# Kernel optimization log

Measured on AMD Instinct MI355X. Metric: run time of the kernel, lower is better.

## Reference

```python
import jax, jax.numpy as jnp
from jax import lax
import numpy as np

# Guide bandwidths (sigma^2) for the cross-bilateral weights.
SIGMA_ALBEDO = 0.01
SIGMA_NORMAL = 0.1
SIGMA_DEPTH = 0.1
EPS = 1e-10

B, H, W = 4, 720, 1280
WIN = 11


def setup_inputs() -> dict:
    key = jax.random.key(0)
    k1, k2, k3, k4 = jax.random.split(key, 4)
    inp = jax.random.normal(k1, (B, 3, H, W), dtype=jnp.float32)
    albedo = jax.random.uniform(k2, (B, 3, H, W), dtype=jnp.float32)
    normal = jax.random.normal(k3, (B, 3, H, W), dtype=jnp.float32)
    normal = normal / (jnp.linalg.norm(normal, axis=1, keepdims=True) + EPS)
    depth = jax.random.uniform(k4, (B, 1, H, W), dtype=jnp.float32)
    return {"input": inp, "albedo": albedo, "normal": normal,
            "depth": depth, "win_size": WIN}


def _cross_bilateral(inp, albedo, normal, depth, win_size):
    pad = win_size // 2
    b, c, h, w = inp.shape

    def pad4(x):
        return jnp.pad(x, ((0, 0), (0, 0), (pad, pad), (pad, pad)), mode="edge")

    ip, ap, np_, dp = pad4(inp), pad4(albedo), pad4(normal), pad4(depth)

    # All (dy, dx) taps in the window, scanned to keep memory O(B*C*H*W).
    offs = jnp.asarray([(dy, dx) for dy in range(win_size) for dx in range(win_size)],
                       dtype=jnp.int32)

    def tap(carry, off):
        acc, wsum = carry
        dy, dx = off[0], off[1]

        def sl(x):
            return lax.dynamic_slice(x, (0, 0, dy, dx), (b, x.shape[1], h, w))

        dA = jnp.sum((albedo - sl(ap)) ** 2, axis=1, keepdims=True)  # [B,1,H,W]
        dN = jnp.sum((normal - sl(np_)) ** 2, axis=1, keepdims=True)
        dD = (depth - sl(dp)) ** 2
        wgt = jnp.exp(-(dA / SIGMA_ALBEDO + dN / SIGMA_NORMAL + dD / SIGMA_DEPTH))
        return (acc + wgt * sl(ip), wsum + wgt), None

    init = (jnp.zeros_like(inp), jnp.zeros((b, 1, h, w), dtype=inp.dtype))
    (acc, wsum), _ = lax.scan(tap, init, offs)
    return acc / jnp.maximum(wsum, EPS)


def reference(input, albedo, normal, depth, win_size):
    return _cross_bilateral(input, albedo, normal, depth, win_size)
```

## Files before the change

### kernel.cpp

```cpp
#include <hip/hip_runtime.h>
#include <math.h>


#define HH   720
#define WW   1280
#define PAD  5
#define WIN  11
#define TW   32
#define TH   16
#define HALO_W (TW + 2 * PAD)
#define HALO_H (TH + 2 * PAD)

typedef _Float16 h2 __attribute__((ext_vector_type(2)));

__device__ __forceinline__ unsigned int pkh2(float a, float b) {
    return __builtin_bit_cast(unsigned int, __builtin_amdgcn_cvt_pkrtz(a, b));
}

__device__ __forceinline__ float dot2acc(h2 d, float acc) {
#if __has_builtin(__builtin_amdgcn_fdot2)
    return __builtin_amdgcn_fdot2(d, d, acc, false);
#else
    float x = (float)d.x, y = (float)d.y;
    return fmaf(x, x, fmaf(y, y, acc));
#endif
}

struct C8 { h2 c0, c1, c2, c3; };

__device__ __forceinline__ C8 unpackC(uint4 g) {
    C8 c;
    c.c0 = __builtin_bit_cast(h2, g.x);
    c.c1 = __builtin_bit_cast(h2, g.y);
    c.c2 = __builtin_bit_cast(h2, g.z);
    c.c3 = __builtin_bit_cast(h2, g.w);
    return c;
}

__device__ __forceinline__ void tap(const C8& c, uint4 g, float4 iv, float4& acc) {
    h2 d0 = __builtin_bit_cast(h2, g.x) - c.c0;
    h2 d1 = __builtin_bit_cast(h2, g.y) - c.c1;
    h2 d2 = __builtin_bit_cast(h2, g.z) - c.c2;
    h2 d3 = __builtin_bit_cast(h2, g.w) - c.c3;
    float e = dot2acc(d0, dot2acc(d1, dot2acc(d2, dot2acc(d3, 0.f))));
    float w = __builtin_amdgcn_exp2f(-e);
    acc.x = fmaf(w, iv.x, acc.x);
    acc.y = fmaf(w, iv.y, acc.y);
    acc.z = fmaf(w, iv.z, acc.z);
    acc.w += w;
}

__global__ __launch_bounds__(256, 4)
void xbilateral_kernel(const float* __restrict__ inp,
                       const float* __restrict__ alb,
                       const float* __restrict__ nrm,
                       const float* __restrict__ dep,
                       float* __restrict__ out)
{
    __shared__ uint4  sG[HALO_H][HALO_W];
    __shared__ float4 sI[HALO_H][HALO_W];

    const int tid = threadIdx.x;
    const int lx  = tid & 31;
    const int ly  = tid >> 5;
    const int bx0 = blockIdx.x * TW;
    const int by0 = blockIdx.y * TH;
    const int b   = blockIdx.z;

    const float kA = 12.01122406f;
    const float kN = 3.79828255f;

    const size_t plane = (size_t)HH * WW;
    const float* albB = alb + (size_t)b * 3 * plane;
    const float* nrmB = nrm + (size_t)b * 3 * plane;
    const float* inpB = inp + (size_t)b * 3 * plane;
    const float* depB = dep + (size_t)b * plane;

    for (int idx = tid; idx < HALO_H * HALO_W; idx += 256) {
        int r = idx / HALO_W;
        int c = idx - r * HALO_W;
        int gy = by0 + r - PAD; gy = min(max(gy, 0), HH - 1);
        int gx = bx0 + c - PAD; gx = min(max(gx, 0), WW - 1);
        size_t o = (size_t)gy * WW + gx;
        float a0 = albB[o], a1 = albB[plane + o], a2 = albB[2 * plane + o];
        float n0 = nrmB[o], n1 = nrmB[plane + o], n2 = nrmB[2 * plane + o];
        float i0 = inpB[o], i1 = inpB[plane + o], i2 = inpB[2 * plane + o];
        float d0 = depB[o];
        sG[r][c] = make_uint4(pkh2(a0 * kA, a1 * kA),
                              pkh2(a2 * kA, d0 * kN),
                              pkh2(n0 * kN, n1 * kN),
                              pkh2(n2 * kN, 0.f));
        sI[r][c] = make_float4(i0, i1, i2, 0.f);
    }
    __syncthreads();

    const int pyA = 2 * ly;
    const C8 cA = unpackC(sG[pyA + PAD][lx + PAD]);
    const C8 cB = unpackC(sG[pyA + 1 + PAD][lx + PAD]);

    float4 accA = make_float4(0.f, 0.f, 0.f, 0.f);
    float4 accB = make_float4(0.f, 0.f, 0.f, 0.f);

    {
        const uint4*  rg = &sG[pyA][lx];
        const float4* ri = &sI[pyA][lx];
#pragma unroll
        for (int dx = 0; dx < WIN; ++dx)
            tap(cA, rg[dx], ri[dx], accA);
    }
    for (int wy = 1; wy <= 10; ++wy) {
        const uint4*  rg = &sG[pyA + wy][lx];
        const float4* ri = &sI[pyA + wy][lx];
#pragma unroll
        for (int dx = 0; dx < WIN; ++dx) {
            uint4  g  = rg[dx];
            float4 iv = ri[dx];
            tap(cA, g, iv, accA);
            tap(cB, g, iv, accB);
        }
    }
    {
        const uint4*  rg = &sG[pyA + 11][lx];
        const float4* ri = &sI[pyA + 11][lx];
#pragma unroll
        for (int dx = 0; dx < WIN; ++dx)
            tap(cB, rg[dx], ri[dx], accB);
    }

    const int ox  = bx0 + lx;
    const int oyA = by0 + pyA;
    const int oyB = oyA + 1;
    float* outB = out + (size_t)b * 3 * plane;
    float invA = 1.0f / fmaxf(accA.w, 1e-10f);
    float invB = 1.0f / fmaxf(accB.w, 1e-10f);
    size_t oA = (size_t)oyA * WW + ox;
    size_t oB = (size_t)oyB * WW + ox;
    outB[oA]             = accA.x * invA;
    outB[plane + oA]     = accA.y * invA;
    outB[2 * plane + oA] = accA.z * invA;
    outB[oB]             = accB.x * invB;
    outB[plane + oB]     = accB.y * invB;
    outB[2 * plane + oB] = accB.z * invB;
}

extern "C" void kernel_launch(void* const* d_in, const int* in_sizes, int n_in,
                              void* d_out, int out_size, void* d_ws, size_t ws_size,
                              hipStream_t stream) {
    const float* inp = (const float*)d_in[0];
    const float* alb = (const float*)d_in[1];
    const float* nrm = (const float*)d_in[2];
    const float* dep = (const float*)d_in[3];
    float* out = (float*)d_out;

    dim3 grid(WW / TW, HH / TH, 4);
    dim3 block(256);
    xbilateral_kernel<<<grid, block, 0, stream>>>(inp, alb, nrm, dep, out);
}
```

Before: 214.9 us.

## Compute four output rows per thread with 32x32 tiles and fp16 input staging

Doubles the tile height to 32 and has each thread compute four vertically adjacent output pixels. Each loaded shared-memory row of guide and input taps is reused across up to four accumulators, which cuts LDS traffic per tap. The input colour is now stored as packed fp16 in LDS, which halves its footprint but reduces the precision of the filtered values. 720 is not a multiple of 32, so the last tile row is partly wasted. The larger register footprint lowers the occupancy target in launch bounds from 4 to 3.

```diff
diff --git a/kernel.cpp b/kernel.cpp
--- a/kernel.cpp
+++ b/kernel.cpp
@@ -7,58 +7,36 @@
 #define PAD  5
 #define WIN  11
 #define TW   32
-#define TH   16
-#define HALO_W (TW + 2 * PAD)
-#define HALO_H (TH + 2 * PAD)
+#define TH   32
+#define HW2  42
 
 typedef _Float16 h2 __attribute__((ext_vector_type(2)));
 
-__device__ __forceinline__ unsigned int pkh2(float a, float b) {
-    return __builtin_bit_cast(unsigned int, __builtin_amdgcn_cvt_pkrtz(a, b));
+__device__ __forceinline__ unsigned pk2(float a, float b) {
+    unsigned lo = __builtin_bit_cast(unsigned short, (_Float16)a);
+    unsigned hi = __builtin_bit_cast(unsigned short, (_Float16)b);
+    return lo | (hi << 16);
 }
 
-__device__ __forceinline__ float dot2acc(h2 d, float acc) {
+__device__ __forceinline__ float fdot2(h2 a, h2 b, float c) {
 #if __has_builtin(__builtin_amdgcn_fdot2)
-    return __builtin_amdgcn_fdot2(d, d, acc, false);
+    return __builtin_amdgcn_fdot2(a, b, c, false);
 #else
-    float x = (float)d.x, y = (float)d.y;
-    return fmaf(x, x, fmaf(y, y, acc));
+    return fmaf((float)a.x, (float)b.x, fmaf((float)a.y, (float)b.y, c));
 #endif
 }
 
-struct C8 { h2 c0, c1, c2, c3; };
+__device__ __forceinline__ h2 bch2(unsigned u) { return __builtin_bit_cast(h2, u); }
 
-__device__ __forceinline__ C8 unpackC(uint4 g) {
-    C8 c;
-    c.c0 = __builtin_bit_cast(h2, g.x);
-    c.c1 = __builtin_bit_cast(h2, g.y);
-    c.c2 = __builtin_bit_cast(h2, g.z);
-    c.c3 = __builtin_bit_cast(h2, g.w);
-    return c;
-}
-
-__device__ __forceinline__ void tap(const C8& c, uint4 g, float4 iv, float4& acc) {
-    h2 d0 = __builtin_bit_cast(h2, g.x) - c.c0;
-    h2 d1 = __builtin_bit_cast(h2, g.y) - c.c1;
-    h2 d2 = __builtin_bit_cast(h2, g.z) - c.c2;
-    h2 d3 = __builtin_bit_cast(h2, g.w) - c.c3;
-    float e = dot2acc(d0, dot2acc(d1, dot2acc(d2, dot2acc(d3, 0.f))));
-    float w = __builtin_amdgcn_exp2f(-e);
-    acc.x = fmaf(w, iv.x, acc.x);
-    acc.y = fmaf(w, iv.y, acc.y);
-    acc.z = fmaf(w, iv.z, acc.z);
-    acc.w += w;
-}
-
-__global__ __launch_bounds__(256, 4)
+__global__ __launch_bounds__(256, 3)
 void xbilateral_kernel(const float* __restrict__ inp,
                        const float* __restrict__ alb,
                        const float* __restrict__ nrm,
                        const float* __restrict__ dep,
                        float* __restrict__ out)
 {
-    __shared__ uint4  sG[HALO_H][HALO_W];
-    __shared__ float4 sI[HALO_H][HALO_W];
+    __shared__ uint4 sG[HW2][HW2];
+    __shared__ uint2 sI[HW2][HW2];
 
     const int tid = threadIdx.x;
     const int lx  = tid & 31;
@@ -76,71 +54,86 @@
     const float* inpB = inp + (size_t)b * 3 * plane;
     const float* depB = dep + (size_t)b * plane;
 
-    for (int idx = tid; idx < HALO_H * HALO_W; idx += 256) {
-        int r = idx / HALO_W;
-        int c = idx - r * HALO_W;
+    for (int idx = tid; idx < HW2 * HW2; idx += 256) {
+        int r = idx / HW2;
+        int c = idx - r * HW2;
         int gy = by0 + r - PAD; gy = min(max(gy, 0), HH - 1);
         int gx = bx0 + c - PAD; gx = min(max(gx, 0), WW - 1);
         size_t o = (size_t)gy * WW + gx;
-        float a0 = albB[o], a1 = albB[plane + o], a2 = albB[2 * plane + o];
-        float n0 = nrmB[o], n1 = nrmB[plane + o], n2 = nrmB[2 * plane + o];
+        float a0 = albB[o] * kA, a1 = albB[plane + o] * kA, a2 = albB[2 * plane + o] * kA;
+        float n0 = nrmB[o] * kN, n1 = nrmB[plane + o] * kN, n2 = nrmB[2 * plane + o] * kN;
+        float d0 = depB[o] * kN;
+        sG[r][c] = make_uint4(pk2(a0, a1), pk2(a2, d0), pk2(n0, n1), pk2(n2, 0.f));
         float i0 = inpB[o], i1 = inpB[plane + o], i2 = inpB[2 * plane + o];
-        float d0 = depB[o];
-        sG[r][c] = make_uint4(pkh2(a0 * kA, a1 * kA),
-                              pkh2(a2 * kA, d0 * kN),
-                              pkh2(n0 * kN, n1 * kN),
-                              pkh2(n2 * kN, 0.f));
-        sI[r][c] = make_float4(i0, i1, i2, 0.f);
+        sI[r][c] = make_uint2(pk2(i0, i1), pk2(i2, 0.f));
     }
     __syncthreads();
 
-    const int pyA = 2 * ly;
-    const C8 cA = unpackC(sG[pyA + PAD][lx + PAD]);
-    const C8 cB = unpackC(sG[pyA + 1 + PAD][lx + PAD]);
+    const int py0 = 4 * ly;
 
-    float4 accA = make_float4(0.f, 0.f, 0.f, 0.f);
-    float4 accB = make_float4(0.f, 0.f, 0.f, 0.f);
+    h2 c0[4], c1[4], c2[4], c3[4];
+#pragma unroll
+    for (int k = 0; k < 4; ++k) {
+        uint4 g = sG[py0 + k + PAD][lx + PAD];
+        c0[k] = bch2(g.x);
+        c1[k] = bch2(g.y);
+        c2[k] = bch2(g.z);
+        c3[k] = bch2(g.w);
+    }
 
-    {
-        const uint4*  rg = &sG[pyA][lx];
-        const float4* ri = &sI[pyA][lx];
+    float4 acc[4];
 #pragma unroll
-        for (int dx = 0; dx < WIN; ++dx)
-            tap(cA, rg[dx], ri[dx], accA);
-    }
-    for (int wy = 1; wy <= 10; ++wy) {
-        const uint4*  rg = &sG[pyA + wy][lx];
-        const float4* ri = &sI[pyA + wy][lx];
+    for (int k = 0; k < 4; ++k) acc[k] = make_float4(0.f, 0.f, 0.f, 0.f);
+
+#pragma unroll 1
+    for (int wy = 0; wy < 14; ++wy) {
+        const uint4* rg = &sG[py0 + wy][lx];
+        const uint2* ri = &sI[py0 + wy][lx];
+        uint4 g[WIN];
+        float v0[WIN], v1[WIN], v2[WIN];
 #pragma unroll
-        for (int dx = 0; dx < WIN; ++dx) {
-            uint4  g  = rg[dx];
-            float4 iv = ri[dx];
-            tap(cA, g, iv, accA);
-            tap(cB, g, iv, accB);
+        for (int d = 0; d < WIN; ++d) g[d] = rg[d];
+#pragma unroll
+        for (int d = 0; d < WIN; ++d) {
+            uint2 t = ri[d];
+            h2 lo = bch2(t.x), hi = bch2(t.y);
+            v0[d] = (float)lo.x;
+            v1[d] = (float)lo.y;
+            v2[d] = (float)hi.x;
+        }
+#pragma unroll
+        for (int k = 0; k < 4; ++k) {
+            if ((unsigned)(wy - k) <= 10u) {
+#pragma unroll
+                for (int d = 0; d < WIN; ++d) {
+                    h2 d0 = bch2(g[d].x) - c0[k];
+                    h2 d1 = bch2(g[d].y) - c1[k];
+                    h2 d2 = bch2(g[d].z) - c2[k];
+                    h2 d3 = bch2(g[d].w) - c3[k];
+                    float e = fdot2(d0, d0, fdot2(d1, d1, fdot2(d2, d2, fdot2(d3, d3, 0.f))));
+                    float w = __builtin_amdgcn_exp2f(-e);
+                    acc[k].x = fmaf(w, v0[d], acc[k].x);
+                    acc[k].y = fmaf(w, v1[d], acc[k].y);
+                    acc[k].z = fmaf(w, v2[d], acc[k].z);
+                    acc[k].w += w;
+                }
+            }
         }
     }
-    {
-        const uint4*  rg = &sG[pyA + 11][lx];
-        const float4* ri = &sI[pyA + 11][lx];
+
+    const int ox = bx0 + lx;
+    float* outB = out + (size_t)b * 3 * plane;
 #pragma unroll
-        for (int dx = 0; dx < WIN; ++dx)
-            tap(cB, rg[dx], ri[dx], accB);
+    for (int k = 0; k < 4; ++k) {
+        int oy = by0 + py0 + k;
+        if (oy < HH) {
+            float inv = 1.0f / fmaxf(acc[k].w, 1e-10f);
+            size_t o = (size_t)oy * WW + ox;
+            outB[o]             = acc[k].x * inv;
+            outB[plane + o]     = acc[k].y * inv;
+            outB[2 * plane + o] = acc[k].z * inv;
+        }
     }
-
-    const int ox  = bx0 + lx;
-    const int oyA = by0 + pyA;
-    const int oyB = oyA + 1;
-    float* outB = out + (size_t)b * 3 * plane;
-    float invA = 1.0f / fmaxf(accA.w, 1e-10f);
-    float invB = 1.0f / fmaxf(accB.w, 1e-10f);
-    size_t oA = (size_t)oyA * WW + ox;
-    size_t oB = (size_t)oyB * WW + ox;
-    outB[oA]             = accA.x * invA;
-    outB[plane + oA]     = accA.y * invA;
-    outB[2 * plane + oA] = accA.z * invA;
-    outB[oB]             = accB.x * invB;
-    outB[plane + oB]     = accB.y * invB;
-    outB[2 * plane + oB] = accB.z * invB;
 }
 
 extern "C" void kernel_launch(void* const* d_in, const int* in_sizes, int n_in,
@@ -152,7 +145,7 @@
     const float* dep = (const float*)d_in[3];
     float* out = (float*)d_out;
 
-    dim3 grid(WW / TW, HH / TH, 4);
+    dim3 grid(WW / TW, (HH + TH - 1) / TH, 4);
     dim3 block(256);
     xbilateral_kernel<<<grid, block, 0, stream>>>(inp, alb, nrm, dep, out);
 }
```

After: 219.4 us. 1.02x slower.
